# Optimization experiments

Measured on AMD Instinct MI355X. Metric: run time of the kernel, lower is better.

The kernel has to match this reference:

```python
import jax, jax.numpy as jnp
import numpy as np

N, L, D = 8, 2048, 128


def setup_inputs() -> dict:
    key = jax.random.key(0)
    k1, k2, k3, k4 = jax.random.split(key, 4)
    x_t = jax.random.normal(k1, (N, L, D), jnp.float32)
    x_f = jax.random.normal(k2, (N, L, D), jnp.float32)
    W = jax.random.normal(k3, (D, D), jnp.float32) / np.sqrt(D)  # proj weight (torch Linear layout)
    b = jax.random.normal(k4, (D,), jnp.float32) * 0.02
    return {"x_t": x_t, "x_f": x_f, "W": W, "b": b}


def _col_score(a, c, scale):
    # softmax attention with zeroed diagonal, then column-sum -> [N, L]
    att = jnp.einsum('nld,nmd->nlm', a, c) * scale
    att = jax.nn.softmax(att, axis=-1)
    att = att * (1.0 - jnp.eye(att.shape[-1], dtype=att.dtype))
    return jnp.sum(att, axis=1)


def _mask(score, time):
    # score: [N, L]; k-th extreme threshold, k = L//2
    k = int(0.5 * score.shape[1])
    if time:
        vals, _ = jax.lax.top_k(score, k)          # k largest, descending
        theta = vals[:, -1:]                        # k-th largest
        return score > theta
    else:
        vals, _ = jax.lax.top_k(-score, k)          # k smallest
        theta = -vals[:, -1:]                       # k-th smallest
        return score <= theta


def reference(x_t, x_f, W, b):
    scale = 1.0 / np.sqrt(W.shape[0])
    pt = x_t @ W.T + b
    pf = x_f @ W.T + b
    score_t = _col_score(pt, pt, scale)
    score_f = _col_score(pf, pf, scale)
    score_tf = _col_score(pt, pf, scale)
    score_ft = _col_score(pf, pt, scale)
    mask_t = _mask(score_t, False)
    mask_f = _mask(score_f, False)
    mask_tf = _mask(score_tf, True)   # computed in original forward (unused in blend)
    mask_ft = _mask(score_ft, True)
    mask_t1 = (mask_t & ~mask_f)[:, :, None]   # [N, L, 1] broadcast over D
    mask_f1 = (mask_f & ~mask_t)[:, :, None]
    x_t1 = jnp.where(mask_t1, x_f, x_t)
    x_f1 = jnp.where(mask_f1, x_t, x_f)
    return (0.5 * (x_t1 + x_t), 0.5 * (x_f1 + x_f))
```

## Files before the change

kernel.cpp:

```cpp
#include <hip/hip_runtime.h>
#include <math.h>

#define LL 2048
#define DD 128
#define NS 16
#define SLAB (LL * DD)
#define SCALE 0.08838834764831845f
#define NT 16
#define NPAIR 136

typedef __attribute__((ext_vector_type(8))) short short8v;
typedef __attribute__((ext_vector_type(4))) float float4v;

__device__ __forceinline__ unsigned int f2bf(float f) {
    unsigned int u = __float_as_uint(f);
    u += 0x7fffu + ((u >> 16) & 1u);
    return u >> 16;
}
__device__ __forceinline__ void pair_decode(int p, int& ib, int& jb) {
    int i = 0;
    while (p >= NT - i) { p -= NT - i; ++i; }
    ib = i; jb = i + p;
}

__device__ __forceinline__ void work_decode(int bx, int by, int& pair, int& ns) {
    const int lin = by * NPAIR + bx;
    const int xcd = lin & 7;
    const int wi  = lin >> 3;
    const int h   = (wi >= NPAIR) ? 1 : 0;
    ns   = xcd + 8 * h;
    pair = wi - NPAIR * h;
}

__device__ __forceinline__ void gl_lds16(const void* g, void* l) {
    __builtin_amdgcn_global_load_lds(
        (const __attribute__((address_space(1))) void*)g,
        (__attribute__((address_space(3))) void*)l, 16, 0, 0);
}

__device__ __forceinline__ void stage_panel(
    const unsigned short* __restrict__ gT, unsigned short* lbuf, int tid)
{
#pragma unroll
    for (int it = 0; it < 2; ++it) {
        const int s   = tid + it * 256;
        const int sb  = (tid & ~63) + it * 256;
        const int row = s >> 2;
        const int oc  = (s & 3) ^ ((row >> 1) & 3);
        gl_lds16(gT + (size_t)row * DD + oc * 8, lbuf + (size_t)sb * 8);
    }
}

__global__ __launch_bounds__(256, 4) void proj_kernel(
    const float* __restrict__ xt, const float* __restrict__ xf,
    const float* __restrict__ W,  const float* __restrict__ bias,
    unsigned short* __restrict__ Ph, unsigned short* __restrict__ Pl)
{
    __shared__ float Alds[64 * 36];
    __shared__ float Blds[128 * 36];
    __shared__ float bs[128];
    const int ns = blockIdx.y;
    const int l0 = blockIdx.x * 64;
    const int src = ns >> 3, n = ns & 7;
    const float* x = (src ? xf : xt) + (size_t)n * LL * DD;
    const int tid = threadIdx.x;
    const int ty = tid >> 4, tx = tid & 15;

    if (tid < 128) bs[tid] = bias[tid];
    __syncthreads();

    float acc[4][8];
#pragma unroll
    for (int i = 0; i < 4; ++i)
#pragma unroll
        for (int j = 0; j < 8; ++j) acc[i][j] = bs[tx + 16 * j];

    for (int kc = 0; kc < 4; ++kc) {
        __syncthreads();
#pragma unroll
        for (int t = 0; t < 2; ++t) {
            int idx = tid + t * 256;
            int r = idx >> 3, k4 = (idx & 7) << 2;
            *(float4*)&Alds[r * 36 + k4] =
                *(const float4*)&x[(size_t)(l0 + r) * DD + kc * 32 + k4];
        }
#pragma unroll
        for (int t = 0; t < 4; ++t) {
            int idx = tid + t * 256;
            int r = idx >> 3, k4 = (idx & 7) << 2;
            *(float4*)&Blds[r * 36 + k4] =
                *(const float4*)&W[(size_t)r * DD + kc * 32 + k4];
        }
        __syncthreads();
#pragma unroll
        for (int k4 = 0; k4 < 32; k4 += 4) {
            float4 a4[4], b4[8];
#pragma unroll
            for (int i = 0; i < 4; ++i) a4[i] = *(const float4*)&Alds[(ty + 16 * i) * 36 + k4];
#pragma unroll
            for (int j = 0; j < 8; ++j) b4[j] = *(const float4*)&Blds[(tx + 16 * j) * 36 + k4];
#pragma unroll
            for (int i = 0; i < 4; ++i)
#pragma unroll
                for (int j = 0; j < 8; ++j) {
                    acc[i][j] = fmaf(a4[i].x, b4[j].x, acc[i][j]);
                    acc[i][j] = fmaf(a4[i].y, b4[j].y, acc[i][j]);
                    acc[i][j] = fmaf(a4[i].z, b4[j].z, acc[i][j]);
                    acc[i][j] = fmaf(a4[i].w, b4[j].w, acc[i][j]);
                }
        }
    }
#pragma unroll
    for (int i = 0; i < 4; ++i) {
        const size_t rowo = (size_t)ns * SLAB + (size_t)(l0 + ty + 16 * i) * DD;
#pragma unroll
        for (int j = 0; j < 8; ++j) {
            float p = acc[i][j];
            unsigned int hb = f2bf(p);
            float hf = __uint_as_float(hb << 16);
            unsigned int lb = f2bf(p - hf);
            Ph[rowo + tx + 16 * j] = (unsigned short)hb;
            Pl[rowo + tx + 16 * j] = (unsigned short)lb;
        }
    }
}

__device__ __forceinline__ void mfma_core(
    const unsigned short* __restrict__ Ph, const unsigned short* __restrict__ Pl,
    int ns, int ib, int jb, int tid,
    unsigned short (*pan)[4096],
    float4v (&acc)[4][4])
{
    const int lane = tid & 63;
    const int quad = lane >> 4, l16 = lane & 15;
    const int wave = tid >> 6;
    const int wr = wave >> 1, wc = wave & 1;
    const bool dg = (ib == jb);

    const unsigned short* sAh = Ph + (size_t)ns * SLAB + (size_t)ib * 128 * DD;
    const unsigned short* sAl = Pl + (size_t)ns * SLAB + (size_t)ib * 128 * DD;
    const unsigned short* sBh = Ph + (size_t)ns * SLAB + (size_t)jb * 128 * DD;
    const unsigned short* sBl = Pl + (size_t)ns * SLAB + (size_t)jb * 128 * DD;

#pragma unroll
    for (int i = 0; i < 4; ++i)
#pragma unroll
        for (int j = 0; j < 4; ++j)
#pragma unroll
            for (int r = 0; r < 4; ++r) acc[i][j][r] = 0.f;

    stage_panel(sAh, pan[0], tid);
    stage_panel(sAl, pan[1], tid);
    if (!dg) {
        stage_panel(sBh, pan[2], tid);
        stage_panel(sBl, pan[3], tid);
    }
    __syncthreads();

#pragma unroll
    for (int kc = 0; kc < 4; ++kc) {
        const int cur = (kc & 1) * 4;
        if (kc < 3) {
            const int nxt = ((kc + 1) & 1) * 4;
            stage_panel(sAh + (kc + 1) * 32, pan[nxt + 0], tid);
            stage_panel(sAl + (kc + 1) * 32, pan[nxt + 1], tid);
            if (!dg) {
                stage_panel(sBh + (kc + 1) * 32, pan[nxt + 2], tid);
                stage_panel(sBl + (kc + 1) * 32, pan[nxt + 3], tid);
            }
        }
        const unsigned short* Ah = pan[cur + 0];
        const unsigned short* Al = pan[cur + 1];
        const unsigned short* Bh = dg ? pan[cur + 0] : pan[cur + 2];
        const unsigned short* Bl = dg ? pan[cur + 1] : pan[cur + 3];

        short8v ah[4], al[4], bh[4], bl[4];
#pragma unroll
        for (int rt = 0; rt < 4; ++rt) {
            const int r = wr * 64 + rt * 16 + l16;
            const int off = r * 32 + ((quad ^ ((r >> 1) & 3)) << 3);
            ah[rt] = *(const short8v*)&Ah[off];
            al[rt] = *(const short8v*)&Al[off];
        }
#pragma unroll
        for (int ct = 0; ct < 4; ++ct) {
            const int r = wc * 64 + ct * 16 + l16;
            const int off = r * 32 + ((quad ^ ((r >> 1) & 3)) << 3);
            bh[ct] = *(const short8v*)&Bh[off];
            bl[ct] = *(const short8v*)&Bl[off];
        }
#pragma unroll
        for (int rt = 0; rt < 4; ++rt)
#pragma unroll
            for (int ct = 0; ct < 4; ++ct) {
                acc[rt][ct] = __builtin_amdgcn_mfma_f32_16x16x32_bf16(ah[rt], bh[ct], acc[rt][ct], 0, 0, 0);
                acc[rt][ct] = __builtin_amdgcn_mfma_f32_16x16x32_bf16(ah[rt], bl[ct], acc[rt][ct], 0, 0, 0);
                acc[rt][ct] = __builtin_amdgcn_mfma_f32_16x16x32_bf16(al[rt], bh[ct], acc[rt][ct], 0, 0, 0);
            }
        if (kc < 3) __syncthreads();
    }
}

__global__ __launch_bounds__(256, 2) void stats_kernel(
    const unsigned short* __restrict__ Ph, const unsigned short* __restrict__ Pl,
    float* __restrict__ Zpart)
{
    __shared__ unsigned short pan[8][4096];
    __shared__ float Zr[128][2], Zc[128][2];
    int pair, ns;  work_decode(blockIdx.x, blockIdx.y, pair, ns);
    int ib, jb;    pair_decode(pair, ib, jb);
    const int tid = threadIdx.x;
    const int lane = tid & 63, quad = lane >> 4, l16 = lane & 15, wave = tid >> 6;
    const int wr = wave >> 1, wc = wave & 1;

    float4v acc[4][4];
    mfma_core(Ph, Pl, ns, ib, jb, tid, pan, acc);

    float cs[4] = {0.f, 0.f, 0.f, 0.f};
#pragma unroll
    for (int rt = 0; rt < 4; ++rt)
#pragma unroll
        for (int rg = 0; rg < 4; ++rg) {
            float e[4];
            float s = 0.f;
#pragma unroll
            for (int ct = 0; ct < 4; ++ct) {
                e[ct] = __expf(acc[rt][ct][rg] * SCALE);
                s += e[ct]; cs[ct] += e[ct];
            }
            s += __shfl_xor(s, 1);
            s += __shfl_xor(s, 2);
            s += __shfl_xor(s, 4);
            s += __shfl_xor(s, 8);
            if (l16 == 0) Zr[wr * 64 + rt * 16 + quad * 4 + rg][wc] = s;
        }

#pragma unroll
    for (int ct = 0; ct < 4; ++ct) {
        float s = cs[ct];
        s += __shfl_xor(s, 16);
        s += __shfl_xor(s, 32);
        if (quad == 0) Zc[wc * 64 + ct * 16 + l16][wr] = s;
    }
    __syncthreads();
    if (tid < 128) {
        Zpart[(ns * 16 + jb) * LL + ib * 128 + tid] = Zr[tid][0] + Zr[tid][1];
        if (ib != jb)
            Zpart[(ns * 16 + ib) * LL + jb * 128 + tid] = Zc[tid][0] + Zc[tid][1];
    }
}

__global__ __launch_bounds__(256) void reduce_stats_kernel(
    const float* __restrict__ Zpart, float* __restrict__ iZfin)
{
    const int idx = blockIdx.x * 256 + threadIdx.x;
    const int ns = idx >> 11, l = idx & 2047;
    float Z = 0.f;
#pragma unroll
    for (int t = 0; t < 16; ++t) Z += Zpart[(ns * 16 + t) * LL + l];
    iZfin[idx] = 1.0f / Z;
}

__global__ __launch_bounds__(256, 2) void colsum_kernel(
    const unsigned short* __restrict__ Ph, const unsigned short* __restrict__ Pl,
    const float* __restrict__ iZfin, float* __restrict__ Spart)
{
    __shared__ unsigned short pan[8][4096];
    __shared__ float Sr[128][2], Sc[128][2];
    int pair, ns;  work_decode(blockIdx.x, blockIdx.y, pair, ns);
    int ib, jb;    pair_decode(pair, ib, jb);
    const int tid = threadIdx.x;
    const int lane = tid & 63, quad = lane >> 4, l16 = lane & 15, wave = tid >> 6;
    const int wr = wave >> 1, wc = wave & 1;

    float4v acc[4][4];
    mfma_core(Ph, Pl, ns, ib, jb, tid, pan, acc);

    float wrow[4][4];
#pragma unroll
    for (int rt = 0; rt < 4; ++rt)
#pragma unroll
        for (int rg = 0; rg < 4; ++rg)
            wrow[rt][rg] = iZfin[ns * LL + ib * 128 + wr * 64 + rt * 16 + quad * 4 + rg];
    float wcol[4];
#pragma unroll
    for (int ct = 0; ct < 4; ++ct)
        wcol[ct] = iZfin[ns * LL + jb * 128 + wc * 64 + ct * 16 + l16];

    float dsum[4] = {0.f, 0.f, 0.f, 0.f};
#pragma unroll
    for (int rt = 0; rt < 4; ++rt)
#pragma unroll
        for (int rg = 0; rg < 4; ++rg) {
            const int rl = wr * 64 + rt * 16 + quad * 4 + rg;
            float ts = 0.f;
#pragma unroll
            for (int ct = 0; ct < 4; ++ct) {
                float e = __expf(acc[rt][ct][rg] * SCALE);
                bool diag = (ib == jb) && (rl == wc * 64 + ct * 16 + l16);
                dsum[ct] += diag ? 0.f : e * wrow[rt][rg];
                ts += e * wcol[ct];
            }
            if (ib != jb) {
                ts += __shfl_xor(ts, 1);
                ts += __shfl_xor(ts, 2);
                ts += __shfl_xor(ts, 4);
                ts += __shfl_xor(ts, 8);
                if (l16 == 0) Sr[rl][wc] = ts;
            }
        }

#pragma unroll
    for (int ct = 0; ct < 4; ++ct) {
        float s = dsum[ct];
        s += __shfl_xor(s, 16);
        s += __shfl_xor(s, 32);
        if (quad == 0) Sc[wc * 64 + ct * 16 + l16][wr] = s;
    }
    __syncthreads();
    if (tid < 128) {
        Spart[((size_t)ns * LL + jb * 128 + tid) * 16 + ib] = Sc[tid][0] + Sc[tid][1];
        if (ib != jb)
            Spart[((size_t)ns * LL + ib * 128 + tid) * 16 + jb] = Sr[tid][0] + Sr[tid][1];
    }
}

__global__ __launch_bounds__(1024) void mask_kernel(
    const float* __restrict__ Spart, unsigned char* __restrict__ maskbuf)
{
    __shared__ double s[LL];
    const int ns = blockIdx.x;
    const int half = blockIdx.y;
    const int tid = threadIdx.x;
#pragma unroll
    for (int h = 0; h < 2; ++h) {
        int m = tid + h * 1024;
        const float* sp = Spart + ((size_t)ns * LL + m) * 16;
        double a = 0.0;
#pragma unroll
        for (int t = 0; t < 16; ++t) a += (double)sp[t];
        s[m] = a;
    }
    __syncthreads();
    const int i = half * 1024 + tid;
    const double si = s[i];
    int cnt = 0;
    for (int j = 0; j < LL; ++j) cnt += (s[j] < si) ? 1 : 0;
    maskbuf[ns * LL + i] = (cnt < 1024) ? 1 : 0;
}

__global__ __launch_bounds__(256) void blend_kernel(
    const float* __restrict__ xt, const float* __restrict__ xf,
    const unsigned char* __restrict__ maskbuf, float* __restrict__ out)
{
    const int idx4 = blockIdx.x * 256 + threadIdx.x;
    const size_t q = (size_t)idx4 * 4;
    const int row = (int)(q >> 7);
    const float4 a = *(const float4*)(xt + q);
    const float4 b = *(const float4*)(xf + q);
    const int mt = maskbuf[row] & 1;
    const int mf = maskbuf[16384 + row] & 1;
    const bool ct = mt && !mf;
    const bool cf = mf && !mt;
    float4 av;
    av.x = 0.5f * (a.x + b.x);  av.y = 0.5f * (a.y + b.y);
    av.z = 0.5f * (a.z + b.z);  av.w = 0.5f * (a.w + b.w);
    float4 o0 = ct ? av : a;
    float4 o1 = cf ? av : b;
    *(float4*)(out + q)                   = o0;
    *(float4*)(out + (size_t)2097152 + q) = o1;
}

extern "C" void kernel_launch(void* const* d_in, const int* in_sizes, int n_in,
                              void* d_out, int out_size, void* d_ws, size_t ws_size,
                              hipStream_t stream)
{
    const float* xt = (const float*)d_in[0];
    const float* xf = (const float*)d_in[1];
    const float* W  = (const float*)d_in[2];
    const float* b  = (const float*)d_in[3];
    float* out = (float*)d_out;

    unsigned short* Ph = (unsigned short*)d_out;
    unsigned short* Pl = Ph + (size_t)NS * SLAB;

    float* Zpart = (float*)d_ws;
    float* iZfin = Zpart + 16 * 16 * LL;
    float* Spart = iZfin + NS * LL;
    unsigned char* maskbuf = (unsigned char*)(Spart + (size_t)16 * LL * 16);

    proj_kernel<<<dim3(32, NS), 256, 0, stream>>>(xt, xf, W, b, Ph, Pl);
    stats_kernel<<<dim3(NPAIR, NS), 256, 0, stream>>>(Ph, Pl, Zpart);
    reduce_stats_kernel<<<128, 256, 0, stream>>>(Zpart, iZfin);
    colsum_kernel<<<dim3(NPAIR, NS), 256, 0, stream>>>(Ph, Pl, iZfin, Spart);
    mask_kernel<<<dim3(NS, 2), 1024, 0, stream>>>(Spart, maskbuf);
    blend_kernel<<<2048, 256, 0, stream>>>(xt, xf, maskbuf, out);
}
```

Measured before the change: 234.0 us.

## Load A-low operand directly to registers, shrink LDS panels, raise occupancy

The A low-part bf16 operand now goes straight from global memory into a double-buffered register array instead of through shared memory. This cuts LDS usage from 8 to 6 panels per block and lets launch bounds request 3 blocks per CU instead of 2. MFMA sections are wrapped in s_setprio to favour the matrix issue. It trades extra VGPRs and uncoalesced global loads for higher occupancy and less LDS traffic. The tighter register budget could cause spills.

```diff
diff --git a/kernel.cpp b/kernel.cpp
--- a/kernel.cpp
+++ b/kernel.cpp
@@ -142,6 +142,11 @@
     const unsigned short* sBh = Ph + (size_t)ns * SLAB + (size_t)jb * 128 * DD;
     const unsigned short* sBl = Pl + (size_t)ns * SLAB + (size_t)jb * 128 * DD;
 
+    const unsigned short* alp[4];
+#pragma unroll
+    for (int rt = 0; rt < 4; ++rt)
+        alp[rt] = sAl + (size_t)(wr * 64 + rt * 16 + l16) * DD + quad * 8;
+
 #pragma unroll
     for (int i = 0; i < 4; ++i)
 #pragma unroll
@@ -150,62 +155,62 @@
             for (int r = 0; r < 4; ++r) acc[i][j][r] = 0.f;
 
     stage_panel(sAh, pan[0], tid);
-    stage_panel(sAl, pan[1], tid);
-    if (!dg) {
-        stage_panel(sBh, pan[2], tid);
-        stage_panel(sBl, pan[3], tid);
-    }
+    if (!dg) stage_panel(sBh, pan[1], tid);
+    stage_panel(sBl, pan[2], tid);
+    short8v alr[2][4];
+#pragma unroll
+    for (int rt = 0; rt < 4; ++rt) alr[0][rt] = *(const short8v*)&alp[rt][0];
     __syncthreads();
 
 #pragma unroll
     for (int kc = 0; kc < 4; ++kc) {
-        const int cur = (kc & 1) * 4;
+        const int cur = (kc & 1) * 3;
         if (kc < 3) {
-            const int nxt = ((kc + 1) & 1) * 4;
+            const int nxt = ((kc + 1) & 1) * 3;
             stage_panel(sAh + (kc + 1) * 32, pan[nxt + 0], tid);
-            stage_panel(sAl + (kc + 1) * 32, pan[nxt + 1], tid);
-            if (!dg) {
-                stage_panel(sBh + (kc + 1) * 32, pan[nxt + 2], tid);
-                stage_panel(sBl + (kc + 1) * 32, pan[nxt + 3], tid);
-            }
-        }
-        const unsigned short* Ah = pan[cur + 0];
-        const unsigned short* Al = pan[cur + 1];
-        const unsigned short* Bh = dg ? pan[cur + 0] : pan[cur + 2];
-        const unsigned short* Bl = dg ? pan[cur + 1] : pan[cur + 3];
-
-        short8v ah[4], al[4], bh[4], bl[4];
+            if (!dg) stage_panel(sBh + (kc + 1) * 32, pan[nxt + 1], tid);
+            stage_panel(sBl + (kc + 1) * 32, pan[nxt + 2], tid);
+#pragma unroll
+            for (int rt = 0; rt < 4; ++rt)
+                alr[(kc + 1) & 1][rt] = *(const short8v*)&alp[rt][(kc + 1) * 32];
+        }
+        const unsigned short* AhP = pan[cur + 0];
+        const unsigned short* BhP = dg ? pan[cur + 0] : pan[cur + 1];
+        const unsigned short* BlP = pan[cur + 2];
+
+        short8v ah[4], bh[4], bl[4];
 #pragma unroll
         for (int rt = 0; rt < 4; ++rt) {
             const int r = wr * 64 + rt * 16 + l16;
             const int off = r * 32 + ((quad ^ ((r >> 1) & 3)) << 3);
-            ah[rt] = *(const short8v*)&Ah[off];
-            al[rt] = *(const short8v*)&Al[off];
+            ah[rt] = *(const short8v*)&AhP[off];
         }
 #pragma unroll
         for (int ct = 0; ct < 4; ++ct) {
             const int r = wc * 64 + ct * 16 + l16;
             const int off = r * 32 + ((quad ^ ((r >> 1) & 3)) << 3);
-            bh[ct] = *(const short8v*)&Bh[off];
-            bl[ct] = *(const short8v*)&Bl[off];
-        }
+            bh[ct] = *(const short8v*)&BhP[off];
+            bl[ct] = *(const short8v*)&BlP[off];
+        }
+        __builtin_amdgcn_s_setprio(1);
 #pragma unroll
         for (int rt = 0; rt < 4; ++rt)
 #pragma unroll
             for (int ct = 0; ct < 4; ++ct) {
                 acc[rt][ct] = __builtin_amdgcn_mfma_f32_16x16x32_bf16(ah[rt], bh[ct], acc[rt][ct], 0, 0, 0);
                 acc[rt][ct] = __builtin_amdgcn_mfma_f32_16x16x32_bf16(ah[rt], bl[ct], acc[rt][ct], 0, 0, 0);
-                acc[rt][ct] = __builtin_amdgcn_mfma_f32_16x16x32_bf16(al[rt], bh[ct], acc[rt][ct], 0, 0, 0);
+                acc[rt][ct] = __builtin_amdgcn_mfma_f32_16x16x32_bf16(alr[kc & 1][rt], bh[ct], acc[rt][ct], 0, 0, 0);
             }
+        __builtin_amdgcn_s_setprio(0);
         if (kc < 3) __syncthreads();
     }
 }
 
-__global__ __launch_bounds__(256, 2) void stats_kernel(
+__global__ __launch_bounds__(256, 3) void stats_kernel(
     const unsigned short* __restrict__ Ph, const unsigned short* __restrict__ Pl,
     float* __restrict__ Zpart)
 {
-    __shared__ unsigned short pan[8][4096];
+    __shared__ unsigned short pan[6][4096];
     __shared__ float Zr[128][2], Zc[128][2];
     int pair, ns;  work_decode(blockIdx.x, blockIdx.y, pair, ns);
     int ib, jb;    pair_decode(pair, ib, jb);
@@ -261,11 +266,11 @@
     iZfin[idx] = 1.0f / Z;
 }
 
-__global__ __launch_bounds__(256, 2) void colsum_kernel(
+__global__ __launch_bounds__(256, 3) void colsum_kernel(
     const unsigned short* __restrict__ Ph, const unsigned short* __restrict__ Pl,
     const float* __restrict__ iZfin, float* __restrict__ Spart)
 {
-    __shared__ unsigned short pan[8][4096];
+    __shared__ unsigned short pan[6][4096];
     __shared__ float Sr[128][2], Sc[128][2];
     int pair, ns;  work_decode(blockIdx.x, blockIdx.y, pair, ns);
     int ib, jb;    pair_decode(pair, ib, jb);
```

Result: no change. 230.3 us (-1.6%).
